# Kernel tuning notes

Hardware: AMD Instinct MI355X
Metric: run time of the kernel (lower is better)

The kernel has to match this reference:

```python
import jax, jax.numpy as jnp
import numpy as np

B, N, D = 8, 2048, 512


def setup_inputs() -> dict:
    key = jax.random.key(0)
    ks = jax.random.split(key, 16)
    s = 1.0 / np.sqrt(D)  # ~ torch Linear default init scale
    inp = {
        "X": jax.random.normal(ks[0], (B, N, D), jnp.float32),
        "Y": jax.random.normal(ks[1], (B, N, D), jnp.float32),
    }
    names = ["xq", "xk", "xv", "yq", "yk", "yv"]
    for i, nm in enumerate(names):
        inp[f"W_{nm}"] = jax.random.uniform(ks[2 + 2 * i], (D, D), jnp.float32, -s, s)
        inp[f"b_{nm}"] = jax.random.uniform(ks[3 + 2 * i], (D,), jnp.float32, -s, s)
    return inp


def _lin(x, W, b):
    # torch nn.Linear: x @ W^T + b
    return jnp.einsum("bnd,ed->bne", x, W) + b


def reference(X, Y, W_xq, b_xq, W_xk, b_xk, W_xv, b_xv, W_yq, b_yq, W_yk, b_yk, W_yv, b_yv):
    d = X.shape[-1]
    scale = 1.0 / jnp.sqrt(jnp.asarray(d, X.dtype))
    Q1, K1, V1 = _lin(X, W_xq, b_xq), _lin(X, W_xk, b_xk), _lin(X, W_xv, b_xv)
    Q2, K2, V2 = _lin(Y, W_yq, b_yq), _lin(Y, W_yk, b_yk), _lin(Y, W_yv, b_yv)
    # NOTE: F.softmax called without dim on a 3-D tensor -> torch legacy dim=0 (batch axis).
    S1 = jnp.einsum("bnd,bmd->bnm", Q1, K2) * scale  # [B, N, N]
    A1 = jax.nn.softmax(S1, axis=0)
    U_A1 = X + jnp.einsum("bnm,bmd->bnd", A1, V2)  # dropout = identity (eval)
    S2 = jnp.einsum("bnd,bmd->bnm", Q2, K1) * scale
    A2 = jax.nn.softmax(S2, axis=0)
    U_A2 = Y + jnp.einsum("bnm,bmd->bnd", A2, V1)
    return U_A1 + U_A2
```

## Files before the change

### kernel.cpp

```cpp
#include <hip/hip_runtime.h>

typedef unsigned short u16;
typedef __attribute__((ext_vector_type(8))) short bf16x8;
typedef __attribute__((ext_vector_type(4))) float f32x4;
typedef __attribute__((ext_vector_type(8))) u16 u16x8;

#define GLOAD_LDS(g, s) __builtin_amdgcn_global_load_lds( \
    (const __attribute__((address_space(1))) void*)(g),   \
    (__attribute__((address_space(3))) void*)(s), 16, 0, 0)

__device__ __forceinline__ u16 f2bf(float f) {
  union { float f; unsigned u; } v; v.f = f;
  unsigned r = v.u + 0x7fffu + ((v.u >> 16) & 1u);
  return (u16)(r >> 16);
}
__device__ __forceinline__ float bf2f(u16 h) {
  union { unsigned u; float f; } v; v.u = ((unsigned)h) << 16;
  return v.f;
}

__device__ __forceinline__ unsigned lds_a(const u16* p) {
  return (unsigned)(unsigned long long)(__attribute__((address_space(3))) const u16*)p;
}
__device__ __forceinline__ bf16x8 ds128(const u16* p) {
  bf16x8 r;
  asm volatile("ds_read_b128 %0, %1" : "=v"(r) : "v"(lds_a(p)));
  return r;
}

__device__ __forceinline__ void stage_pair(const u16* gA, int lda, const u16* gB, int ldb,
                                           u16* lA, u16* lB, int wave, int lane) {
  int row = (wave << 4) + (lane >> 2);
  int kb  = (lane & 3) << 3;
  GLOAD_LDS(gA + row * lda + kb,        lA + (wave << 9));
  GLOAD_LDS(gA + (row + 64) * lda + kb, lA + ((wave + 4) << 9));
  GLOAD_LDS(gB + row * ldb + kb,        lB + (wave << 9));
  GLOAD_LDS(gB + (row + 64) * ldb + kb, lB + ((wave + 4) << 9));
}

__device__ __forceinline__ void gemm_seg(f32x4 (&acc)[4][4],
    const u16* Ag, const u16* Bg, int lda, int ldb, int nk,
    u16* As, u16* Bs, int wave, int lane) {
  const int wr = (wave >> 1) << 6, wc = (wave & 1) << 6;
  const int rl = lane & 15, rk = (lane >> 4) << 3;
  stage_pair(Ag, lda, Bg, ldb, As, Bs, wave, lane);
  if (nk > 1)
    stage_pair(Ag + 32, lda, Bg + 32, ldb, As + 4096, Bs + 4096, wave, lane);
  int bufsel = 0;
  for (int kt = 0; kt < nk; ++kt) {
    if (kt + 1 < nk) asm volatile("s_waitcnt vmcnt(4)" ::: "memory");
    else             asm volatile("s_waitcnt vmcnt(0)" ::: "memory");
    __builtin_amdgcn_s_barrier();
    asm volatile("" ::: "memory");
    if (kt + 2 < nk) {
      int nb = bufsel + 2; if (nb >= 3) nb -= 3;
      stage_pair(Ag + (long)(kt + 2) * 32, lda, Bg + (long)(kt + 2) * 32, ldb,
                 As + nb * 4096, Bs + nb * 4096, wave, lane);
    }
    const u16* ab = As + bufsel * 4096;
    const u16* bb = Bs + bufsel * 4096;
    bf16x8 af[4], bfr[4];
#pragma unroll
    for (int i = 0; i < 4; i++)
      af[i]  = *(const bf16x8*)(ab + ((wr + (i << 4) + rl) << 5) + rk);
#pragma unroll
    for (int j = 0; j < 4; j++)
      bfr[j] = *(const bf16x8*)(bb + ((wc + (j << 4) + rl) << 5) + rk);
#pragma unroll
    for (int i = 0; i < 4; i++)
#pragma unroll
      for (int j = 0; j < 4; j++)
        acc[i][j] = __builtin_amdgcn_mfma_f32_16x16x32_bf16(af[i], bfr[j], acc[i][j], 0, 0, 0);
    __builtin_amdgcn_sched_barrier(0);
    bufsel = bufsel + 1; if (bufsel == 3) bufsel = 0;
  }
}


__device__ __forceinline__ void stage128(const u16* gA, int lda, const u16* gB, int ldb,
                                         u16* Ad, u16* Bd, int tid) {
  int rw = tid >> 3;
  int gs = ((tid & 7) ^ (rw & 7)) << 3;
  int wb = (tid >> 6) << 9;
#pragma unroll
  for (int p = 0; p < 4; p++) {
    GLOAD_LDS(gA + (long)(p * 32 + rw) * lda + gs, Ad + p * 2048 + wb);
    GLOAD_LDS(gB + (long)(p * 32 + rw) * ldb + gs, Bd + p * 2048 + wb);
  }
}

__device__ __forceinline__ void gemm128(f32x4 (&acc)[4][4],
    const u16* Ag, int lda, const u16* Bg, int ldb, int nk,
    u16* As, u16* Bs, int tid) {
  const int lane = tid & 63, wid = tid >> 6;
  const int wr = (wid >> 1) << 6, wc = (wid & 1) << 6;
  const int rl = lane & 15, kg = lane >> 4;
  const int swz0 = (kg ^ (rl & 7)) << 3;
  const int rbA = (wr + rl) * 64, rbB = (wc + rl) * 64;

  stage128(Ag, lda, Bg, ldb, As, Bs, tid);
  asm volatile("s_waitcnt vmcnt(0)" ::: "memory");
  __builtin_amdgcn_s_barrier();
  for (int t = 0; t < nk; ++t) {
    if (t + 1 < nk)
      stage128(Ag + (t + 1) * 64, lda, Bg + (t + 1) * 64, ldb,
               As + ((t + 1) & 1) * 8192, Bs + ((t + 1) & 1) * 8192, tid);
    const u16* ab = As + (t & 1) * 8192 + rbA;
    const u16* bb = Bs + (t & 1) * 8192 + rbB;
    bf16x8 a0[4], b0[4], a1[4], b1[4];
#pragma unroll
    for (int i = 0; i < 4; i++) a0[i] = ds128(ab + i * 1024 + swz0);
#pragma unroll
    for (int j = 0; j < 4; j++) b0[j] = ds128(bb + j * 1024 + swz0);
#pragma unroll
    for (int i = 0; i < 4; i++) a1[i] = ds128(ab + i * 1024 + (swz0 ^ 32));
#pragma unroll
    for (int j = 0; j < 4; j++) b1[j] = ds128(bb + j * 1024 + (swz0 ^ 32));
    asm volatile("s_waitcnt lgkmcnt(8)" ::: "memory");
    __builtin_amdgcn_sched_barrier(0);
    __builtin_amdgcn_s_setprio(1);
#pragma unroll
    for (int i = 0; i < 4; i++)
#pragma unroll
      for (int j = 0; j < 4; j++)
        acc[i][j] = __builtin_amdgcn_mfma_f32_16x16x32_bf16(a0[i], b0[j], acc[i][j], 0, 0, 0);
    __builtin_amdgcn_s_setprio(0);
    asm volatile("s_waitcnt lgkmcnt(0)" ::: "memory");
    __builtin_amdgcn_sched_barrier(0);
    __builtin_amdgcn_s_setprio(1);
#pragma unroll
    for (int i = 0; i < 4; i++)
#pragma unroll
      for (int j = 0; j < 4; j++)
        acc[i][j] = __builtin_amdgcn_mfma_f32_16x16x32_bf16(a1[i], b1[j], acc[i][j], 0, 0, 0);
    __builtin_amdgcn_s_setprio(0);
    __builtin_amdgcn_sched_barrier(0);
    if (t + 1 < nk) asm volatile("s_waitcnt vmcnt(0)" ::: "memory");
    __builtin_amdgcn_s_barrier();
  }
}

__global__ __launch_bounds__(256) void k_cvt2(const float* __restrict__ inX,
                                              const float* __restrict__ inY,
                                              u16* __restrict__ oX, u16* __restrict__ oY,
                                              int n8) {
  int i = blockIdx.x * 256 + threadIdx.x;
  const float* in = (i < n8) ? inX : inY;
  u16* out = (i < n8) ? oX : oY;
  int k = (i < n8) ? i : i - n8;
  const float4* pf = (const float4*)in + (long)k * 2;
  float4 a = pf[0], b = pf[1];
  u16x8 o;
  o[0] = f2bf(a.x); o[1] = f2bf(a.y); o[2] = f2bf(a.z); o[3] = f2bf(a.w);
  o[4] = f2bf(b.x); o[5] = f2bf(b.y); o[6] = f2bf(b.z); o[7] = f2bf(b.w);
  *((u16x8*)out + k) = o;
}

struct P6 { const float* p[6]; };
struct O6 { u16* p[6]; };

__global__ __launch_bounds__(256) void k_cvt_w(P6 w, u16* __restrict__ out) {
  int z = blockIdx.y;
  int i = blockIdx.x * 256 + threadIdx.x;
  const float4* pf = (const float4*)w.p[z] + (long)i * 2;
  float4 a = pf[0], b = pf[1];
  u16x8 o;
  o[0] = f2bf(a.x); o[1] = f2bf(a.y); o[2] = f2bf(a.z); o[3] = f2bf(a.w);
  o[4] = f2bf(b.x); o[5] = f2bf(b.y); o[6] = f2bf(b.z); o[7] = f2bf(b.w);
  *((u16x8*)(out + (long)z * 262144) + i) = o;
}

__global__ __launch_bounds__(256) void k_proj(const u16* __restrict__ Xb, const u16* __restrict__ Yb,
                                              const u16* __restrict__ Wb, P6 bias, O6 dst) {
  __shared__ u16 As[12288], Bs[12288];
  int x = blockIdx.x;
  int swz = (x & 7) * 384 + (x >> 3);
  int bm = swz / 24;
  int r  = swz - bm * 24;
  int z = r >> 2, bn = r & 3;
  int tid = threadIdx.x, wave = tid >> 6, lane = tid & 63;
  const u16* Ag = (z < 3 ? Xb : Yb) + (long)bm * 128 * 512;
  const u16* Bg = Wb + (long)z * 262144 + (long)bn * 128 * 512;
  f32x4 acc[4][4] = {};
  gemm_seg(acc, Ag, Bg, 512, 512, 16, As, Bs, wave, lane);
  const float* bi = bias.p[z];
  u16* D = dst.p[z];
  int wr = (wave >> 1) << 6, wc = (wave & 1) << 6;
  int row0 = bm * 128 + wr + ((lane >> 4) << 2);
  int col0 = bn * 128 + wc + (lane & 15);
  float bj[4];
#pragma unroll
  for (int j = 0; j < 4; j++) bj[j] = bi[col0 + (j << 4)];
#pragma unroll
  for (int i = 0; i < 4; i++)
#pragma unroll
    for (int j = 0; j < 4; j++)
#pragma unroll
      for (int rr = 0; rr < 4; rr++)
        D[(long)(row0 + (i << 4) + rr) * 512 + col0 + (j << 4)] = f2bf(acc[i][j][rr] + bj[j]);
}

__global__ __launch_bounds__(256) void k_s(const u16* __restrict__ Q, const u16* __restrict__ K,
                                           u16* __restrict__ S) {
  __shared__ u16 As[16384], Bs[16384];
  int x = blockIdx.x;
  int swz = (x & 7) * 256 + (x >> 3);
  int bn = swz & 15, bm = (swz >> 4) & 15, b = swz >> 8;
  int tid = threadIdx.x;
  const u16* Ag = Q + (long)b * 1048576 + (long)bm * 128 * 512;
  const u16* Bg = K + (long)b * 1048576 + (long)bn * 128 * 512;
  f32x4 acc[4][4] = {};
  gemm128(acc, Ag, 512, Bg, 512, 8, As, Bs, tid);
  u16* D = S + (long)b * 4194304;
  const float scale = 0.04419417382415922f;
  int lane = tid & 63, wid = tid >> 6;
  int wr = (wid >> 1) << 6, wc = (wid & 1) << 6;
  int row0 = bm * 128 + wr + ((lane >> 4) << 2);
  int col0 = bn * 128 + wc + (lane & 15);
#pragma unroll
  for (int i = 0; i < 4; i++)
#pragma unroll
    for (int j = 0; j < 4; j++)
#pragma unroll
      for (int rr = 0; rr < 4; rr++)
        D[(long)(row0 + (i << 4) + rr) * 2048 + col0 + (j << 4)] = f2bf(acc[i][j][rr] * scale);
}

__global__ __launch_bounds__(256) void k_softmax(u16* __restrict__ S) {
  int idx = blockIdx.x * 256 + threadIdx.x;
  u16x8 v[8];
#pragma unroll
  for (int b = 0; b < 8; b++) v[b] = *((const u16x8*)(S + (long)b * 4194304) + idx);
#pragma unroll
  for (int j = 0; j < 8; j++) {
    float e[8], m = -1e30f;
#pragma unroll
    for (int b = 0; b < 8; b++) { e[b] = bf2f(v[b][j]); m = fmaxf(m, e[b]); }
    float s = 0.f;
#pragma unroll
    for (int b = 0; b < 8; b++) { e[b] = __expf(e[b] - m); s += e[b]; }
    float inv = 1.0f / s;
#pragma unroll
    for (int b = 0; b < 8; b++) v[b][j] = f2bf(e[b] * inv);
  }
#pragma unroll
  for (int b = 0; b < 8; b++) *((u16x8*)(S + (long)b * 4194304) + idx) = v[b];
}

__global__ __launch_bounds__(256) void k_tr(const u16* __restrict__ V1, const u16* __restrict__ V2,
                                            u16* __restrict__ T1, u16* __restrict__ T2) {
  __shared__ u16 tile[64][65];
  int z = blockIdx.z;
  const u16* src = (z < 8 ? V1 : V2) + (long)(z & 7) * 1048576;
  u16*       dst = (z < 8 ? T1 : T2) + (long)(z & 7) * 1048576;
  int n0 = blockIdx.x * 64, d0 = blockIdx.y * 64;
  int t = threadIdx.x;
  int r = t >> 2, cs = (t & 3) * 16;
  const u16x8* sp = (const u16x8*)(src + (long)(n0 + r) * 512 + d0 + cs);
  u16x8 a = sp[0], b = sp[1];
#pragma unroll
  for (int jj = 0; jj < 8; jj++) { tile[r][cs + jj] = a[jj]; tile[r][cs + 8 + jj] = b[jj]; }
  __syncthreads();
  u16x8 o0, o1;
#pragma unroll
  for (int jj = 0; jj < 8; jj++) { o0[jj] = tile[cs + jj][r]; o1[jj] = tile[cs + 8 + jj][r]; }
  u16x8* op = (u16x8*)(dst + (long)(d0 + r) * 2048 + n0 + cs);
  op[0] = o0; op[1] = o1;
}

__global__ __launch_bounds__(256) void k_pv(const u16* __restrict__ A, const u16* __restrict__ Vt,
                                            const float* __restrict__ X, const float* __restrict__ Y,
                                            float* __restrict__ out, int mode) {
  __shared__ u16 As[16384], Bs[16384];
  int x = blockIdx.x;
  int swz = (x & 7) * 64 + (x >> 3);
  int bn = swz & 3, bm = (swz >> 2) & 15, b = swz >> 6;
  int tid = threadIdx.x;
  const u16* Ag = A + (long)b * 4194304 + (long)bm * 128 * 2048;
  const u16* Bg = Vt + (long)b * 1048576 + (long)bn * 128 * 2048;
  f32x4 acc[4][4] = {};
  gemm128(acc, Ag, 2048, Bg, 2048, 32, As, Bs, tid);
  int lane = tid & 63, wid = tid >> 6;
  int wr = (wid >> 1) << 6, wc = (wid & 1) << 6;
  int row0 = bm * 128 + wr + ((lane >> 4) << 2);
  int col0 = bn * 128 + wc + (lane & 15);
  long base = (long)b * 1048576;
#pragma unroll
  for (int i = 0; i < 4; i++)
#pragma unroll
    for (int j = 0; j < 4; j++)
#pragma unroll
      for (int rr = 0; rr < 4; rr++) {
        long idx = base + (long)(row0 + (i << 4) + rr) * 512 + col0 + (j << 4);
        float v = acc[i][j][rr];
        out[idx] = mode ? (out[idx] + v) : (v + X[idx] + Y[idx]);
      }
}

extern "C" void kernel_launch(void* const* d_in, const int* in_sizes, int n_in,
                              void* d_out, int out_size, void* d_ws, size_t ws_size,
                              hipStream_t stream) {
  const float* X = (const float*)d_in[0];
  const float* Y = (const float*)d_in[1];
  P6 wp, bp;
  for (int i = 0; i < 6; i++) { wp.p[i] = (const float*)d_in[2 + 2 * i]; bp.p[i] = (const float*)d_in[3 + 2 * i]; }

  const long NX = 8L * 2048 * 512;
  const long NS = 8L * 2048 * 2048;
  u16* p = (u16*)d_ws;
  u16* Xb = p;  p += NX;
  u16* Yb = p;  p += NX;
  u16* Wb = p;  p += 6L * 512 * 512;
  u16* Q1 = p;  p += NX;
  u16* K2 = p;  p += NX;
  u16* Q2 = p;  p += NX;
  u16* K1 = p;  p += NX;
  u16* Sb = p;  p += NS;
  u16* V1 = Sb;
  u16* V2 = Sb + NX;
  u16* Vt1 = Xb;
  u16* Vt2 = Yb;
  (void)ws_size; (void)in_sizes; (void)n_in; (void)out_size;

  dim3 T(256);
  k_cvt2<<<dim3(8192), T, 0, stream>>>(X, Y, Xb, Yb, (int)(NX / 8));
  k_cvt_w<<<dim3(128, 6), T, 0, stream>>>(wp, Wb);
  O6 dst; dst.p[0] = Q1; dst.p[1] = K1; dst.p[2] = V1; dst.p[3] = Q2; dst.p[4] = K2; dst.p[5] = V2;
  k_proj<<<dim3(3072), T, 0, stream>>>(Xb, Yb, Wb, bp, dst);
  k_tr<<<dim3(32, 8, 16), T, 0, stream>>>(V1, V2, Vt1, Vt2);
  k_s<<<dim3(2048), T, 0, stream>>>(Q2, K1, Sb);
  k_softmax<<<dim3(2048), T, 0, stream>>>(Sb);
  k_pv<<<dim3(512), T, 0, stream>>>(Sb, Vt1, X, Y, (float*)d_out, 0);
  k_s<<<dim3(2048), T, 0, stream>>>(Q1, K2, Sb);
  k_softmax<<<dim3(2048), T, 0, stream>>>(Sb);
  k_pv<<<dim3(512), T, 0, stream>>>(Sb, Vt2, X, Y, (float*)d_out, 1);
}
```

Before: 367.6 us.

## Use 256x256 GEMM tiles with 512 threads and split-K for PV

```diff
diff --git a/kernel.cpp b/kernel.cpp
--- a/kernel.cpp
+++ b/kernel.cpp
@@ -77,66 +77,60 @@
 }
 
 
-__device__ __forceinline__ void stage128(const u16* gA, int lda, const u16* gB, int ldb,
-                                         u16* Ad, u16* Bd, int tid) {
+__device__ __forceinline__ void stage256sq(const u16* gA, int lda, const u16* gB, int ldb,
+                                           u16* Ad, u16* Bd, int tid) {
   int rw = tid >> 3;
   int gs = ((tid & 7) ^ (rw & 7)) << 3;
   int wb = (tid >> 6) << 9;
 #pragma unroll
   for (int p = 0; p < 4; p++) {
-    GLOAD_LDS(gA + (long)(p * 32 + rw) * lda + gs, Ad + p * 2048 + wb);
-    GLOAD_LDS(gB + (long)(p * 32 + rw) * ldb + gs, Bd + p * 2048 + wb);
+    GLOAD_LDS(gA + (long)(p * 64 + rw) * lda + gs, Ad + p * 4096 + wb);
+    GLOAD_LDS(gB + (long)(p * 64 + rw) * ldb + gs, Bd + p * 4096 + wb);
   }
 }
 
-__device__ __forceinline__ void gemm128(f32x4 (&acc)[4][4],
+__device__ __forceinline__ void gemm256sq(f32x4 (&acc)[8][4],
     const u16* Ag, int lda, const u16* Bg, int ldb, int nk,
     u16* As, u16* Bs, int tid) {
   const int lane = tid & 63, wid = tid >> 6;
-  const int wr = (wid >> 1) << 6, wc = (wid & 1) << 6;
+  const int wr = (wid >> 2) << 7;
+  const int wc = (wid & 3) << 6;
   const int rl = lane & 15, kg = lane >> 4;
   const int swz0 = (kg ^ (rl & 7)) << 3;
   const int rbA = (wr + rl) * 64, rbB = (wc + rl) * 64;
 
-  stage128(Ag, lda, Bg, ldb, As, Bs, tid);
+  stage256sq(Ag, lda, Bg, ldb, As, Bs, tid);
   asm volatile("s_waitcnt vmcnt(0)" ::: "memory");
   __builtin_amdgcn_s_barrier();
   for (int t = 0; t < nk; ++t) {
     if (t + 1 < nk)
-      stage128(Ag + (t + 1) * 64, lda, Bg + (t + 1) * 64, ldb,
-               As + ((t + 1) & 1) * 8192, Bs + ((t + 1) & 1) * 8192, tid);
-    const u16* ab = As + (t & 1) * 8192 + rbA;
-    const u16* bb = Bs + (t & 1) * 8192 + rbB;
-    bf16x8 a0[4], b0[4], a1[4], b1[4];
-#pragma unroll
-    for (int i = 0; i < 4; i++) a0[i] = ds128(ab + i * 1024 + swz0);
-#pragma unroll
-    for (int j = 0; j < 4; j++) b0[j] = ds128(bb + j * 1024 + swz0);
-#pragma unroll
-    for (int i = 0; i < 4; i++) a1[i] = ds128(ab + i * 1024 + (swz0 ^ 32));
-#pragma unroll
-    for (int j = 0; j < 4; j++) b1[j] = ds128(bb + j * 1024 + (swz0 ^ 32));
-    asm volatile("s_waitcnt lgkmcnt(8)" ::: "memory");
-    __builtin_amdgcn_sched_barrier(0);
-    __builtin_amdgcn_s_setprio(1);
-#pragma unroll
-    for (int i = 0; i < 4; i++)
-#pragma unroll
-      for (int j = 0; j < 4; j++)
-        acc[i][j] = __builtin_amdgcn_mfma_f32_16x16x32_bf16(a0[i], b0[j], acc[i][j], 0, 0, 0);
-    __builtin_amdgcn_s_setprio(0);
-    asm volatile("s_waitcnt lgkmcnt(0)" ::: "memory");
-    __builtin_amdgcn_sched_barrier(0);
-    __builtin_amdgcn_s_setprio(1);
-#pragma unroll
-    for (int i = 0; i < 4; i++)
-#pragma unroll
-      for (int j = 0; j < 4; j++)
-        acc[i][j] = __builtin_amdgcn_mfma_f32_16x16x32_bf16(a1[i], b1[j], acc[i][j], 0, 0, 0);
-    __builtin_amdgcn_s_setprio(0);
-    __builtin_amdgcn_sched_barrier(0);
-    if (t + 1 < nk) asm volatile("s_waitcnt vmcnt(0)" ::: "memory");
-    __builtin_amdgcn_s_barrier();
+      stage256sq(Ag + (t + 1) * 64, lda, Bg + (t + 1) * 64, ldb,
+                 As + ((t + 1) & 1) * 16384, Bs + ((t + 1) & 1) * 16384, tid);
+    const u16* ab = As + (t & 1) * 16384 + rbA;
+    const u16* bb = Bs + (t & 1) * 16384 + rbB;
+#pragma unroll
+    for (int kk = 0; kk < 2; kk++) {
+      const int sw = swz0 ^ (kk << 5);
+      bf16x8 a[8], b[4];
+#pragma unroll
+      for (int i = 0; i < 8; i++) a[i] = ds128(ab + i * 1024 + sw);
+#pragma unroll
+      for (int j = 0; j < 4; j++) b[j] = ds128(bb + j * 1024 + sw);
+      asm volatile("s_waitcnt lgkmcnt(0)" ::: "memory");
+      __builtin_amdgcn_sched_barrier(0);
+      __builtin_amdgcn_s_setprio(1);
+#pragma unroll
+      for (int i = 0; i < 8; i++)
+#pragma unroll
+        for (int j = 0; j < 4; j++)
+          acc[i][j] = __builtin_amdgcn_mfma_f32_16x16x32_bf16(a[i], b[j], acc[i][j], 0, 0, 0);
+      __builtin_amdgcn_s_setprio(0);
+      __builtin_amdgcn_sched_barrier(0);
+    }
+    if (t + 1 < nk) {
+      asm volatile("s_waitcnt vmcnt(0)" ::: "memory");
+      __builtin_amdgcn_s_barrier();
+    }
   }
 }
 
@@ -200,25 +194,24 @@
         D[(long)(row0 + (i << 4) + rr) * 512 + col0 + (j << 4)] = f2bf(acc[i][j][rr] + bj[j]);
 }
 
-__global__ __launch_bounds__(256) void k_s(const u16* __restrict__ Q, const u16* __restrict__ K,
+__global__ __launch_bounds__(512) void k_s(const u16* __restrict__ Q, const u16* __restrict__ K,
                                            u16* __restrict__ S) {
-  __shared__ u16 As[16384], Bs[16384];
+  __shared__ u16 As[32768], Bs[32768];
   int x = blockIdx.x;
-  int swz = (x & 7) * 256 + (x >> 3);
-  int bn = swz & 15, bm = (swz >> 4) & 15, b = swz >> 8;
+  int swz = (x & 7) * 64 + (x >> 3);
+  int bn = swz & 7, bm = (swz >> 3) & 7, b = swz >> 6;
   int tid = threadIdx.x;
-  const u16* Ag = Q + (long)b * 1048576 + (long)bm * 128 * 512;
-  const u16* Bg = K + (long)b * 1048576 + (long)bn * 128 * 512;
-  f32x4 acc[4][4] = {};
-  gemm128(acc, Ag, 512, Bg, 512, 8, As, Bs, tid);
+  const u16* Ag = Q + (long)b * 1048576 + (long)bm * 256 * 512;
+  const u16* Bg = K + (long)b * 1048576 + (long)bn * 256 * 512;
+  f32x4 acc[8][4] = {};
+  gemm256sq(acc, Ag, 512, Bg, 512, 8, As, Bs, tid);
   u16* D = S + (long)b * 4194304;
   const float scale = 0.04419417382415922f;
   int lane = tid & 63, wid = tid >> 6;
-  int wr = (wid >> 1) << 6, wc = (wid & 1) << 6;
-  int row0 = bm * 128 + wr + ((lane >> 4) << 2);
-  int col0 = bn * 128 + wc + (lane & 15);
-#pragma unroll
-  for (int i = 0; i < 4; i++)
+  int row0 = bm * 256 + ((wid >> 2) << 7) + ((lane >> 4) << 2);
+  int col0 = bn * 256 + ((wid & 3) << 6) + (lane & 15);
+#pragma unroll
+  for (int i = 0; i < 8; i++)
 #pragma unroll
     for (int j = 0; j < 4; j++)
 #pragma unroll
@@ -268,33 +261,43 @@
   op[0] = o0; op[1] = o1;
 }
 
-__global__ __launch_bounds__(256) void k_pv(const u16* __restrict__ A, const u16* __restrict__ Vt,
+__global__ __launch_bounds__(512) void k_pv(const u16* __restrict__ A, const u16* __restrict__ Vt,
                                             const float* __restrict__ X, const float* __restrict__ Y,
-                                            float* __restrict__ out, int mode) {
-  __shared__ u16 As[16384], Bs[16384];
+                                            float* __restrict__ out, float* __restrict__ P,
+                                            int mode) {
+  __shared__ u16 As[32768], Bs[32768];
   int x = blockIdx.x;
-  int swz = (x & 7) * 64 + (x >> 3);
-  int bn = swz & 3, bm = (swz >> 2) & 15, b = swz >> 6;
+  int swz = (x & 7) * 32 + (x >> 3);
+  int kc = swz & 1, bn = (swz >> 1) & 1, bm = (swz >> 2) & 7, b = swz >> 5;
   int tid = threadIdx.x;
-  const u16* Ag = A + (long)b * 4194304 + (long)bm * 128 * 2048;
-  const u16* Bg = Vt + (long)b * 1048576 + (long)bn * 128 * 2048;
-  f32x4 acc[4][4] = {};
-  gemm128(acc, Ag, 2048, Bg, 2048, 32, As, Bs, tid);
+  const u16* Ag = A + (long)b * 4194304 + (long)bm * 256 * 2048 + kc * 1024;
+  const u16* Bg = Vt + (long)b * 1048576 + (long)bn * 256 * 2048 + kc * 1024;
+  f32x4 acc[8][4] = {};
+  gemm256sq(acc, Ag, 2048, Bg, 2048, 16, As, Bs, tid);
   int lane = tid & 63, wid = tid >> 6;
-  int wr = (wid >> 1) << 6, wc = (wid & 1) << 6;
-  int row0 = bm * 128 + wr + ((lane >> 4) << 2);
-  int col0 = bn * 128 + wc + (lane & 15);
+  int row0 = bm * 256 + ((wid >> 2) << 7) + ((lane >> 4) << 2);
+  int col0 = bn * 256 + ((wid & 3) << 6) + (lane & 15);
   long base = (long)b * 1048576;
-#pragma unroll
-  for (int i = 0; i < 4; i++)
+  float* D = kc ? P : out;
+#pragma unroll
+  for (int i = 0; i < 8; i++)
 #pragma unroll
     for (int j = 0; j < 4; j++)
 #pragma unroll
       for (int rr = 0; rr < 4; rr++) {
         long idx = base + (long)(row0 + (i << 4) + rr) * 512 + col0 + (j << 4);
         float v = acc[i][j][rr];
-        out[idx] = mode ? (out[idx] + v) : (v + X[idx] + Y[idx]);
+        if (mode) D[idx] += v;
+        else      D[idx] = kc ? v : (v + X[idx] + Y[idx]);
       }
+}
+
+__global__ __launch_bounds__(256) void k_fin(float* __restrict__ out, const float* __restrict__ P) {
+  long i = (long)(blockIdx.x * 256 + threadIdx.x) * 4;
+  float4 o = *(const float4*)(out + i);
+  float4 p = *(const float4*)(P + i);
+  o.x += p.x; o.y += p.y; o.z += p.z; o.w += p.w;
+  *(float4*)(out + i) = o;
 }
 
 extern "C" void kernel_launch(void* const* d_in, const int* in_sizes, int n_in,
@@ -320,6 +323,7 @@
   u16* V2 = Sb + NX;
   u16* Vt1 = Xb;
   u16* Vt2 = Yb;
+  float* Pbuf = (float*)Q2;
   (void)ws_size; (void)in_sizes; (void)n_in; (void)out_size;
 
   dim3 T(256);
@@ -328,10 +332,11 @@
   O6 dst; dst.p[0] = Q1; dst.p[1] = K1; dst.p[2] = V1; dst.p[3] = Q2; dst.p[4] = K2; dst.p[5] = V2;
   k_proj<<<dim3(3072), T, 0, stream>>>(Xb, Yb, Wb, bp, dst);
   k_tr<<<dim3(32, 8, 16), T, 0, stream>>>(V1, V2, Vt1, Vt2);
-  k_s<<<dim3(2048), T, 0, stream>>>(Q2, K1, Sb);
+  k_s<<<dim3(512), dim3(512), 0, stream>>>(Q2, K1, Sb);
   k_softmax<<<dim3(2048), T, 0, stream>>>(Sb);
-  k_pv<<<dim3(512), T, 0, stream>>>(Sb, Vt1, X, Y, (float*)d_out, 0);
-  k_s<<<dim3(2048), T, 0, stream>>>(Q1, K2, Sb);
+  k_pv<<<dim3(256), dim3(512), 0, stream>>>(Sb, Vt1, X, Y, (float*)d_out, Pbuf, 0);
+  k_s<<<dim3(512), dim3(512), 0, stream>>>(Q1, K2, Sb);
   k_softmax<<<dim3(2048), T, 0, stream>>>(Sb);
-  k_pv<<<dim3(512), T, 0, stream>>>(Sb, Vt2, X, Y, (float*)d_out, 1);
-}
+  k_pv<<<dim3(256), dim3(512), 0, stream>>>(Sb, Vt2, X, Y, (float*)d_out, Pbuf, 1);
+  k_fin<<<dim3((int)(NX / 1024)), T, 0, stream>>>((float*)d_out, Pbuf);
+}
```

Measured after the change: 408.4 us. 11.1% more time.
